# Performance work log

Hardware: AMD Instinct MI355X
Metric: run time of the kernel (lower is better)

The kernel has to match this reference:

```python
import jax, jax.numpy as jnp
import numpy as np

B, T, O = 64, 2048, 3          # batch, window_len, overlap (O >= ngram_n-1)
D, V = 512, 128                # embed_dim, vocab_size
M, NG, H = 100000, 4, 4        # engram memory_size, ngram_n, engram/sgrm num_heads
HD = D // H                    # head_dim = 128
PAD = 0
EPS_RMS = 1e-6


def _engram_primes():
    # per-head rolling-hash primes, exactly as in MultiHeadEngram.setup
    ps = []
    base = 131
    for h in range(H):
        x = base + h * 1009
        row = []
        for _ in range(NG):
            row.append(x)
            x = x * 31 + 1
        ps.append(row)
    return jnp.asarray(np.array(ps, dtype=np.uint32))  # (H, NG)


def setup_inputs() -> dict:
    key = jax.random.key(0)
    ks = jax.random.split(key, 10)
    tokens_w = jax.random.randint(ks[0], (B, T), 0, V, dtype=jnp.int32)
    prev_ids_overlap = jax.random.randint(ks[1], (B, O), 0, V, dtype=jnp.int32)
    mask_bool = jax.random.randint(ks[2], (B, T), 0, 2) > 0
    embed_table = jax.random.normal(ks[3], (V, D), jnp.float32) * 0.02
    engram_table = jax.random.normal(ks[4], (M, H, HD), jnp.float32) * 0.02
    gate_logit = jnp.full((H, HD), -2.0, jnp.float32)
    temp = jnp.ones((H,), jnp.float32)
    sal_W = jax.random.normal(ks[5], (D, H), jnp.float32) * 0.02
    sal_b = jnp.zeros((H,), jnp.float32)
    gate_W = jax.random.normal(ks[6], (HD, 1), jnp.float32) * 0.02
    gate_b = jnp.zeros((1,), jnp.float32)
    rms_scale = jnp.ones((D,), jnp.float32)
    return {"tokens_w": tokens_w, "prev_ids_overlap": prev_ids_overlap,
            "mask_bool": mask_bool, "embed_table": embed_table,
            "engram_table": engram_table, "gate_logit": gate_logit,
            "temp": temp, "sal_W": sal_W, "sal_b": sal_b,
            "gate_W": gate_W, "gate_b": gate_b, "rms_scale": rms_scale}


def reference(tokens_w, prev_ids_overlap, mask_bool, embed_table, engram_table,
              gate_logit, temp, sal_W, sal_b, gate_W, gate_b, rms_scale):
    # ---- MultiHeadEngram: hashed n-gram multi-head gather + sigmoid gate ----
    cur = jnp.where(tokens_w == PAD, 0, tokens_w)
    prv = jnp.where(prev_ids_overlap == PAD, 0, prev_ids_overlap)
    full_seq = jnp.concatenate([prv, cur], axis=1).astype(jnp.uint32)  # (B, O+T)
    primes = _engram_primes()                                          # (H, NG)
    hash_sums = jnp.zeros((B, T, H), dtype=jnp.uint32)
    for i in range(NG):  # rolling n-gram hash (uint32 wraparound)
        chunk = full_seq[:, O - i: O + T - i]                          # (B, T)
        hash_sums = hash_sums + chunk[:, :, None] * primes[None, None, :, i]
    lookup = (hash_sums % M).astype(jnp.int32)                         # (B, T, H)
    # per-head gather: row lookup[b,t,h] of head h's table slice
    retrieved = engram_table[lookup, jnp.arange(H)[None, None, :], :]  # (B, T, H, HD)
    gate = jax.nn.sigmoid(gate_logit)                                  # (H, HD)
    engram_out = (retrieved * gate[None, None]).reshape(B, T, D)

    # token embedding + engram injection (dropout is identity: deterministic)
    x = embed_table[tokens_w] + engram_out                             # (B, T, D)

    # ---- SalienceWriteHead: masked softmax temporal pooling + gating ----
    x_heads = x.reshape(B, T, H, HD)
    temperature = jax.nn.softplus(temp) + 0.3                          # (H,)
    logits = (x @ sal_W + sal_b) / temperature[None, None, :]          # (B, T, H)
    m = mask_bool[:, :, None]
    safe_logits = jnp.where(m, logits, -1e9)
    max_logits = jax.lax.stop_gradient(jnp.max(safe_logits, axis=1, keepdims=True))
    exps = jnp.where(m, jnp.exp(safe_logits - max_logits), 0.0)
    weights = exps / (jnp.sum(exps, axis=1, keepdims=True) + 1e-6)     # (B, T, H)
    write_vec_heads = jnp.einsum('bth,bthd->bhd', weights, x_heads)    # (B, H, HD)
    gate_logits = write_vec_heads @ gate_W + gate_b                    # (B, H, 1)
    window_valid = jnp.any(mask_bool, axis=1)[:, None, None]
    write_u_heads = jax.nn.sigmoid(gate_logits) * window_valid.astype(jnp.float32)
    write_vec = write_vec_heads.reshape(B, D)
    # RMSNorm
    rms = jnp.sqrt(jnp.mean(jnp.square(write_vec), axis=-1, keepdims=True) + EPS_RMS)
    write_vec = write_vec / rms * rms_scale
    write_u_expanded = jnp.tile(write_u_heads, (1, 1, HD)).reshape(B, D)
    return jnp.concatenate([write_vec, write_u_expanded], axis=-1)     # (B, 2D)
```

## Files before the change

### kernel.cpp

```cpp
#include <hip/hip_runtime.h>
#include <stdint.h>

#define B_ 64
#define T_ 2048
#define O_ 3
#define D_ 512
#define M_ 100000
#define H_ 4
#define HD_ 128
#define TC_ 128
#define NCH_ (T_ / TC_)
#define PSTR_ 132

__device__ __constant__ unsigned PRIMES_c[H_][4] = {
  {131u,  4062u,  125923u, 3903614u},
  {1140u, 35341u, 1095572u, 33962733u},
  {2149u, 66620u, 2065221u, 64021852u},
  {3158u, 97899u, 3034870u, 94080971u},
};

template<int CTRL, int RMASK>
__device__ __forceinline__ float dpp_term(float x) {
  return __int_as_float(__builtin_amdgcn_update_dpp(
      0, __float_as_int(x), CTRL, RMASK, 0xF, true));
}

__device__ __forceinline__ float red32(float x) {
  x += dpp_term<0xB1, 0xF>(x);
  x += dpp_term<0x4E, 0xF>(x);
  x += dpp_term<0x141, 0xF>(x);
  x += dpp_term<0x140, 0xF>(x);
  x += __shfl_xor(x, 16, 64);
  return x;
}

__device__ __forceinline__ float wave_sum(float x) {
  x += dpp_term<0xB1, 0xF>(x);
  x += dpp_term<0x4E, 0xF>(x);
  x += dpp_term<0x141, 0xF>(x);
  x += dpp_term<0x140, 0xF>(x);
  x += dpp_term<0x142, 0xA>(x);
  x += dpp_term<0x143, 0xC>(x);
  return __int_as_float(__builtin_amdgcn_readlane(__float_as_int(x), 63));
}

__device__ __forceinline__ bool read_mask(const void* mb, size_t i, int imode) {
  return imode ? (((const int*)mb)[i] != 0)
               : (((const unsigned char*)mb)[i] != 0);
}

__device__ __forceinline__ void detect_imode(const void* maskbuf, int tid,
                                             int* s_imode) {
  if (tid < 64) {
    const uint4* mw = (const uint4*)maskbuf;
    unsigned bad = 0;
    #pragma unroll
    for (int i = 0; i < 8; ++i) {
      uint4 v = mw[tid + i * 64];
      bad |= (v.x > 1u) | (v.y > 1u) | (v.z > 1u) | (v.w > 1u);
    }
    unsigned long long anybad = __ballot(bad != 0);
    if (tid == 0) *s_imode = (anybad == 0ull) ? 1 : 0;
  }
}

__global__ __launch_bounds__(256) void k_pass1(
    const int* __restrict__ tokens, const int* __restrict__ prev,
    const void* __restrict__ maskbuf, const float* __restrict__ embed,
    const float* __restrict__ engram, const float* __restrict__ gate_logit,
    const float* __restrict__ temp, const float* __restrict__ salW,
    const float* __restrict__ salb, float* __restrict__ partials)
{
  int blk = blockIdx.x;
  int b = blk / NCH_, c = blk % NCH_;
  int t0 = c * TC_;
  int tid = threadIdx.x;
  int h = tid >> 6, lane = tid & 63;
  int half = lane >> 5, sl = lane & 31;

  __shared__ int s_imode;
  __shared__ int ltok[TC_ + 3];
  __shared__ unsigned eoff[TC_ * H_];
  __shared__ int s_act[TC_];
  __shared__ int s_cnt2[2];
  __shared__ int s_nact;

  detect_imode(maskbuf, tid, &s_imode);
  for (int j = tid; j < TC_ + 3; j += 256) {
    int g = t0 + j;
    ltok[j] = (g < O_) ? prev[b * O_ + g] : tokens[(size_t)b * T_ + g - O_];
  }
  __syncthreads();

  int imode = s_imode;
  bool act = false;
  unsigned long long bal = 0;
  if (tid < TC_) {
    act = read_mask(maskbuf, (size_t)b * T_ + t0 + tid, imode);
    bal = __ballot(act);
    if ((tid & 63) == 0) s_cnt2[tid >> 6] = __popcll(bal);
  }
  __syncthreads();
  if (tid < TC_) {
    int l = tid & 63;
    int pre = __popcll(bal & ((1ull << l) - 1));
    int base = (tid >> 6) ? s_cnt2[0] : 0;
    if (act) s_act[base + pre] = tid;
    if (tid == 0) s_nact = s_cnt2[0] + s_cnt2[1];
  }
  __syncthreads();
  int nact = s_nact;

  for (int k = tid; k < nact * H_; k += 256) {
    int a  = k >> 2;
    int hh = k & 3;
    int j  = s_act[a];
    unsigned hs = (unsigned)ltok[j + 3] * PRIMES_c[hh][0]
                + (unsigned)ltok[j + 2] * PRIMES_c[hh][1]
                + (unsigned)ltok[j + 1] * PRIMES_c[hh][2]
                + (unsigned)ltok[j]     * PRIMES_c[hh][3];
    unsigned idx = hs % (unsigned)M_;
    eoff[k] = idx * (unsigned)(H_ * HD_) + (unsigned)(hh * HD_);
  }
  __syncthreads();

  int d0 = sl * 4;
  int gd = h * HD_ + d0;
  float4 glv = *(const float4*)(gate_logit + gd);
  float g0 = 1.f / (1.f + __expf(-glv.x));
  float g1 = 1.f / (1.f + __expf(-glv.y));
  float g2 = 1.f / (1.f + __expf(-glv.z));
  float g3 = 1.f / (1.f + __expf(-glv.w));
  float w0 = salW[(gd + 0) * H_ + h];
  float w1 = salW[(gd + 1) * H_ + h];
  float w2 = salW[(gd + 2) * H_ + h];
  float w3 = salW[(gd + 3) * H_ + h];
  float tv = temp[h];
  float sp = (tv > 20.f) ? tv : log1pf(__expf(tv));
  float invT = 1.f / (sp + 0.3f);
  float sb = salb[h];

  float m = -1e30f, s = 0.f;
  float a0 = 0.f, a1 = 0.f, a2 = 0.f, a3 = 0.f;

  for (int k = 0; k < nact; k += 4) {
    int ka = k + half, kb = k + 2 + half;
    bool va = ka < nact, vb = kb < nact;
    int ia = va ? ka : 0;
    int ib = vb ? kb : 0;
    int ja = s_act[ia], jb = s_act[ib];
    unsigned eoa = eoff[ia * H_ + h], eob = eoff[ib * H_ + h];
    int ta = ltok[ja + 3], tb = ltok[jb + 3];
    float4 ra = *(const float4*)(engram + eoa + d0);
    float4 rb = *(const float4*)(engram + eob + d0);
    float4 ea = *(const float4*)(embed + ta * D_ + gd);
    float4 eb = *(const float4*)(embed + tb * D_ + gd);
    float xa0 = fmaf(ra.x, g0, ea.x);
    float xa1 = fmaf(ra.y, g1, ea.y);
    float xa2 = fmaf(ra.z, g2, ea.z);
    float xa3 = fmaf(ra.w, g3, ea.w);
    float xb0 = fmaf(rb.x, g0, eb.x);
    float xb1 = fmaf(rb.y, g1, eb.y);
    float xb2 = fmaf(rb.z, g2, eb.z);
    float xb3 = fmaf(rb.w, g3, eb.w);
    float pda = fmaf(xa3, w3, fmaf(xa2, w2, fmaf(xa1, w1, xa0 * w0)));
    float pdb = fmaf(xb3, w3, fmaf(xb2, w2, fmaf(xb1, w1, xb0 * w0)));
    float da = red32(pda);
    float db = red32(pdb);
    float la = va ? (da + sb) * invT : -1e30f;
    float lb = vb ? (db + sb) * invT : -1e30f;
    float nm = fmaxf(m, fmaxf(la, lb));
    float al = __expf(m - nm);
    float wa = __expf(la - nm);
    float wb = __expf(lb - nm);
    s  = fmaf(s,  al, wa + wb);
    a0 = fmaf(a0, al, fmaf(wa, xa0, wb * xb0));
    a1 = fmaf(a1, al, fmaf(wa, xa1, wb * xb1));
    a2 = fmaf(a2, al, fmaf(wa, xa2, wb * xb2));
    a3 = fmaf(a3, al, fmaf(wa, xa3, wb * xb3));
    m = nm;
  }

  float pm = __shfl_xor(m, 32, 64);
  float M2 = fmaxf(m, pm);
  float fs = __expf(m - M2);
  float fp = __expf(pm - M2);
  float S2 = fmaf(s, fs, __shfl_xor(s, 32, 64) * fp);
  float A0 = fmaf(a0, fs, __shfl_xor(a0, 32, 64) * fp);
  float A1 = fmaf(a1, fs, __shfl_xor(a1, 32, 64) * fp);
  float A2 = fmaf(a2, fs, __shfl_xor(a2, 32, 64) * fp);
  float A3 = fmaf(a3, fs, __shfl_xor(a3, 32, 64) * fp);

  float* P = partials + ((size_t)(b * NCH_ + c) * H_ + h) * PSTR_;
  if (half == 0) {
    *(float4*)(P + d0) = make_float4(A0, A1, A2, A3);
    if (sl == 0) { P[HD_] = M2; P[HD_ + 1] = S2; }
  }
}

__global__ __launch_bounds__(256) void k_pass2(
    const float* __restrict__ partials, const void* __restrict__ maskbuf,
    const float* __restrict__ gateW, const float* __restrict__ gateb,
    const float* __restrict__ rms_scale, float* __restrict__ out)
{
  int b = blockIdx.x;
  int tid = threadIdx.x, h = tid >> 6, lane = tid & 63;

  __shared__ int s_imode;
  __shared__ float s_ss[H_];
  detect_imode(maskbuf, tid, &s_imode);
  __syncthreads();

  int d0 = lane * 2;
  const float* Pb = partials + (size_t)b * NCH_ * H_ * PSTR_;
  float M = -1e30f;
  for (int cc = 0; cc < NCH_; ++cc)
    M = fmaxf(M, Pb[(cc * H_ + h) * PSTR_ + HD_]);
  float S = 0.f, B0 = 0.f, B1 = 0.f;
  for (int cc = 0; cc < NCH_; ++cc) {
    const float* Pc = Pb + (cc * H_ + h) * PSTR_;
    float f = __expf(Pc[HD_] - M);
    float2 a = *(const float2*)(Pc + d0);
    S  = fmaf(Pc[HD_ + 1], f, S);
    B0 = fmaf(a.x, f, B0);
    B1 = fmaf(a.y, f, B1);
  }
  float inv = 1.f / (S + 1e-6f);
  float v0 = B0 * inv, v1 = B1 * inv;

  float pg = v0 * gateW[d0] + v1 * gateW[d0 + 1];
  float ss = v0 * v0 + v1 * v1;
  float gl  = wave_sum(pg);
  float sst = wave_sum(ss);
  if (lane == 0) s_ss[h] = sst;
  __syncthreads();
  float tot = s_ss[0] + s_ss[1] + s_ss[2] + s_ss[3];
  float rinv = rsqrtf(tot / (float)D_ + 1e-6f);
  float anyf = (S > 0.5f) ? 1.f : 0.f;
  float u = (1.f / (1.f + __expf(-(gl + gateb[0])))) * anyf;

  int gd = h * HD_ + d0;
  size_t ob = (size_t)b * (2 * D_);
  out[ob + gd]          = v0 * rinv * rms_scale[gd];
  out[ob + gd + 1]      = v1 * rinv * rms_scale[gd + 1];
  out[ob + D_ + gd]     = u;
  out[ob + D_ + gd + 1] = u;
}

extern "C" void kernel_launch(void* const* d_in, const int* in_sizes, int n_in,
                              void* d_out, int out_size, void* d_ws, size_t ws_size,
                              hipStream_t stream)
{
  const int*   tokens     = (const int*)d_in[0];
  const int*   prev       = (const int*)d_in[1];
  const void*  mask       = d_in[2];
  const float* embed      = (const float*)d_in[3];
  const float* engram     = (const float*)d_in[4];
  const float* gate_logit = (const float*)d_in[5];
  const float* temp       = (const float*)d_in[6];
  const float* salW       = (const float*)d_in[7];
  const float* salb       = (const float*)d_in[8];
  const float* gateW      = (const float*)d_in[9];
  const float* gateb      = (const float*)d_in[10];
  const float* rms_scale  = (const float*)d_in[11];
  float* out = (float*)d_out;

  float* partials = (float*)d_ws;

  k_pass1<<<B_ * NCH_, 256, 0, stream>>>(
      tokens, prev, mask, embed, engram, gate_logit, temp, salW, salb,
      partials);
  k_pass2<<<B_, 256, 0, stream>>>(
      partials, mask, gateW, gateb, rms_scale, out);
}
```

Measured before the change: 286.8 us.

## Halve chunk size and gather four engram rows per half-wave per iteration

Chunks shrink from 128 to 64 tokens, which doubles the number of pass-1 blocks. Mask compaction now runs in a single wave with one ballot, and the current token ids are compacted into shared memory. The main loop handles four active tokens per half-wave instead of two, so more independent gathers from the engram and embed tables are in flight to hide latency. Pass 2 no longer redundantly detects the mask format. In exchange, the partials buffer and the pass-2 merge double in size, and the mask is speculatively read as int even when it is byte-typed, which reads up to four times past the byte range.

```diff
diff --git a/kernel.cpp b/kernel.cpp
--- a/kernel.cpp
+++ b/kernel.cpp
@@ -8,7 +8,7 @@
 #define M_ 100000
 #define H_ 4
 #define HD_ 128
-#define TC_ 128
+#define TC_ 64
 #define NCH_ (T_ / TC_)
 #define PSTR_ 132
 
@@ -42,11 +42,6 @@
   x += dpp_term<0x142, 0xA>(x);
   x += dpp_term<0x143, 0xC>(x);
   return __int_as_float(__builtin_amdgcn_readlane(__float_as_int(x), 63));
-}
-
-__device__ __forceinline__ bool read_mask(const void* mb, size_t i, int imode) {
-  return imode ? (((const int*)mb)[i] != 0)
-               : (((const unsigned char*)mb)[i] != 0);
 }
 
 __device__ __forceinline__ void detect_imode(const void* maskbuf, int tid,
@@ -81,46 +76,44 @@
   __shared__ int s_imode;
   __shared__ int ltok[TC_ + 3];
   __shared__ unsigned eoff[TC_ * H_];
+  __shared__ int ltokc[TC_];
   __shared__ int s_act[TC_];
-  __shared__ int s_cnt2[2];
   __shared__ int s_nact;
 
   detect_imode(maskbuf, tid, &s_imode);
-  for (int j = tid; j < TC_ + 3; j += 256) {
-    int g = t0 + j;
-    ltok[j] = (g < O_) ? prev[b * O_ + g] : tokens[(size_t)b * T_ + g - O_];
-  }
-  __syncthreads();
-
-  int imode = s_imode;
-  bool act = false;
-  unsigned long long bal = 0;
+  if (tid < TC_ + 3) {
+    int g = t0 + tid;
+    ltok[tid] = (g < O_) ? prev[b * O_ + g] : tokens[(size_t)b * T_ + g - O_];
+  }
+  bool act_i = false, act_b = false;
   if (tid < TC_) {
-    act = read_mask(maskbuf, (size_t)b * T_ + t0 + tid, imode);
-    bal = __ballot(act);
-    if ((tid & 63) == 0) s_cnt2[tid >> 6] = __popcll(bal);
-  }
-  __syncthreads();
-  if (tid < TC_) {
-    int l = tid & 63;
-    int pre = __popcll(bal & ((1ull << l) - 1));
-    int base = (tid >> 6) ? s_cnt2[0] : 0;
-    if (act) s_act[base + pre] = tid;
-    if (tid == 0) s_nact = s_cnt2[0] + s_cnt2[1];
+    size_t mi = (size_t)b * T_ + t0 + tid;
+    act_i = ((const int*)maskbuf)[mi] != 0;
+    act_b = ((const unsigned char*)maskbuf)[mi] != 0;
+  }
+  __syncthreads();
+
+  if (tid < 64) {
+    bool act = s_imode ? act_i : act_b;
+    unsigned long long bal = __ballot(act);
+    int pre = __popcll(bal & ((1ull << tid) - 1));
+    if (act) s_act[pre] = tid;
+    if (tid == 0) s_nact = __popcll(bal);
   }
   __syncthreads();
   int nact = s_nact;
 
-  for (int k = tid; k < nact * H_; k += 256) {
-    int a  = k >> 2;
-    int hh = k & 3;
+  if (tid < nact * H_) {
+    int a  = tid >> 2;
+    int hh = tid & 3;
     int j  = s_act[a];
     unsigned hs = (unsigned)ltok[j + 3] * PRIMES_c[hh][0]
                 + (unsigned)ltok[j + 2] * PRIMES_c[hh][1]
                 + (unsigned)ltok[j + 1] * PRIMES_c[hh][2]
                 + (unsigned)ltok[j]     * PRIMES_c[hh][3];
     unsigned idx = hs % (unsigned)M_;
-    eoff[k] = idx * (unsigned)(H_ * HD_) + (unsigned)(hh * HD_);
+    eoff[tid] = idx * (unsigned)(H_ * HD_) + (unsigned)(hh * HD_);
+    if (hh == 0) ltokc[a] = ltok[j + 3];
   }
   __syncthreads();
 
@@ -141,43 +134,67 @@
   float sb = salb[h];
 
   float m = -1e30f, s = 0.f;
-  float a0 = 0.f, a1 = 0.f, a2 = 0.f, a3 = 0.f;
-
-  for (int k = 0; k < nact; k += 4) {
-    int ka = k + half, kb = k + 2 + half;
-    bool va = ka < nact, vb = kb < nact;
-    int ia = va ? ka : 0;
-    int ib = vb ? kb : 0;
-    int ja = s_act[ia], jb = s_act[ib];
-    unsigned eoa = eoff[ia * H_ + h], eob = eoff[ib * H_ + h];
-    int ta = ltok[ja + 3], tb = ltok[jb + 3];
-    float4 ra = *(const float4*)(engram + eoa + d0);
-    float4 rb = *(const float4*)(engram + eob + d0);
-    float4 ea = *(const float4*)(embed + ta * D_ + gd);
-    float4 eb = *(const float4*)(embed + tb * D_ + gd);
-    float xa0 = fmaf(ra.x, g0, ea.x);
-    float xa1 = fmaf(ra.y, g1, ea.y);
-    float xa2 = fmaf(ra.z, g2, ea.z);
-    float xa3 = fmaf(ra.w, g3, ea.w);
-    float xb0 = fmaf(rb.x, g0, eb.x);
-    float xb1 = fmaf(rb.y, g1, eb.y);
-    float xb2 = fmaf(rb.z, g2, eb.z);
-    float xb3 = fmaf(rb.w, g3, eb.w);
-    float pda = fmaf(xa3, w3, fmaf(xa2, w2, fmaf(xa1, w1, xa0 * w0)));
-    float pdb = fmaf(xb3, w3, fmaf(xb2, w2, fmaf(xb1, w1, xb0 * w0)));
-    float da = red32(pda);
-    float db = red32(pdb);
-    float la = va ? (da + sb) * invT : -1e30f;
-    float lb = vb ? (db + sb) * invT : -1e30f;
-    float nm = fmaxf(m, fmaxf(la, lb));
-    float al = __expf(m - nm);
-    float wa = __expf(la - nm);
-    float wb = __expf(lb - nm);
-    s  = fmaf(s,  al, wa + wb);
-    a0 = fmaf(a0, al, fmaf(wa, xa0, wb * xb0));
-    a1 = fmaf(a1, al, fmaf(wa, xa1, wb * xb1));
-    a2 = fmaf(a2, al, fmaf(wa, xa2, wb * xb2));
-    a3 = fmaf(a3, al, fmaf(wa, xa3, wb * xb3));
+  float4 acc = make_float4(0.f, 0.f, 0.f, 0.f);
+
+  for (int k = 0; k < nact; k += 8) {
+    int bse = k + half * 4;
+    bool v0 = bse + 0 < nact;
+    bool v1 = bse + 1 < nact;
+    bool v2 = bse + 2 < nact;
+    bool v3 = bse + 3 < nact;
+    int j0 = v0 ? bse + 0 : 0;
+    int j1 = v1 ? bse + 1 : 0;
+    int j2 = v2 ? bse + 2 : 0;
+    int j3 = v3 ? bse + 3 : 0;
+    unsigned e0 = eoff[j0 * H_ + h];
+    unsigned e1 = eoff[j1 * H_ + h];
+    unsigned e2 = eoff[j2 * H_ + h];
+    unsigned e3 = eoff[j3 * H_ + h];
+    int c0 = ltokc[j0], c1 = ltokc[j1], c2 = ltokc[j2], c3 = ltokc[j3];
+    float4 r0 = *(const float4*)(engram + e0 + d0);
+    float4 r1 = *(const float4*)(engram + e1 + d0);
+    float4 r2 = *(const float4*)(engram + e2 + d0);
+    float4 r3 = *(const float4*)(engram + e3 + d0);
+    float4 q0 = *(const float4*)(embed + c0 * D_ + gd);
+    float4 q1 = *(const float4*)(embed + c1 * D_ + gd);
+    float4 q2 = *(const float4*)(embed + c2 * D_ + gd);
+    float4 q3 = *(const float4*)(embed + c3 * D_ + gd);
+    float4 x0v, x1v, x2v, x3v;
+    x0v.x = fmaf(r0.x, g0, q0.x); x0v.y = fmaf(r0.y, g1, q0.y);
+    x0v.z = fmaf(r0.z, g2, q0.z); x0v.w = fmaf(r0.w, g3, q0.w);
+    x1v.x = fmaf(r1.x, g0, q1.x); x1v.y = fmaf(r1.y, g1, q1.y);
+    x1v.z = fmaf(r1.z, g2, q1.z); x1v.w = fmaf(r1.w, g3, q1.w);
+    x2v.x = fmaf(r2.x, g0, q2.x); x2v.y = fmaf(r2.y, g1, q2.y);
+    x2v.z = fmaf(r2.z, g2, q2.z); x2v.w = fmaf(r2.w, g3, q2.w);
+    x3v.x = fmaf(r3.x, g0, q3.x); x3v.y = fmaf(r3.y, g1, q3.y);
+    x3v.z = fmaf(r3.z, g2, q3.z); x3v.w = fmaf(r3.w, g3, q3.w);
+    float pd0 = fmaf(x0v.w, w3, fmaf(x0v.z, w2, fmaf(x0v.y, w1, x0v.x * w0)));
+    float pd1 = fmaf(x1v.w, w3, fmaf(x1v.z, w2, fmaf(x1v.y, w1, x1v.x * w0)));
+    float pd2 = fmaf(x2v.w, w3, fmaf(x2v.z, w2, fmaf(x2v.y, w1, x2v.x * w0)));
+    float pd3 = fmaf(x3v.w, w3, fmaf(x3v.z, w2, fmaf(x3v.y, w1, x3v.x * w0)));
+    float dt0 = red32(pd0);
+    float dt1 = red32(pd1);
+    float dt2 = red32(pd2);
+    float dt3 = red32(pd3);
+    float l0 = v0 ? (dt0 + sb) * invT : -1e30f;
+    float l1 = v1 ? (dt1 + sb) * invT : -1e30f;
+    float l2 = v2 ? (dt2 + sb) * invT : -1e30f;
+    float l3 = v3 ? (dt3 + sb) * invT : -1e30f;
+    float nm = fmaxf(fmaxf(fmaxf(l0, l1), fmaxf(l2, l3)), m);
+    float al  = __expf(m  - nm);
+    float u0 = __expf(l0 - nm);
+    float u1 = __expf(l1 - nm);
+    float u2 = __expf(l2 - nm);
+    float u3 = __expf(l3 - nm);
+    s = fmaf(s, al, (u0 + u1) + (u2 + u3));
+    acc.x = fmaf(acc.x, al,
+        fmaf(u3, x3v.x, fmaf(u2, x2v.x, fmaf(u1, x1v.x, u0 * x0v.x))));
+    acc.y = fmaf(acc.y, al,
+        fmaf(u3, x3v.y, fmaf(u2, x2v.y, fmaf(u1, x1v.y, u0 * x0v.y))));
+    acc.z = fmaf(acc.z, al,
+        fmaf(u3, x3v.z, fmaf(u2, x2v.z, fmaf(u1, x1v.z, u0 * x0v.z))));
+    acc.w = fmaf(acc.w, al,
+        fmaf(u3, x3v.w, fmaf(u2, x2v.w, fmaf(u1, x1v.w, u0 * x0v.w))));
     m = nm;
   }
 
@@ -186,10 +203,10 @@
   float fs = __expf(m - M2);
   float fp = __expf(pm - M2);
   float S2 = fmaf(s, fs, __shfl_xor(s, 32, 64) * fp);
-  float A0 = fmaf(a0, fs, __shfl_xor(a0, 32, 64) * fp);
-  float A1 = fmaf(a1, fs, __shfl_xor(a1, 32, 64) * fp);
-  float A2 = fmaf(a2, fs, __shfl_xor(a2, 32, 64) * fp);
-  float A3 = fmaf(a3, fs, __shfl_xor(a3, 32, 64) * fp);
+  float A0 = fmaf(acc.x, fs, __shfl_xor(acc.x, 32, 64) * fp);
+  float A1 = fmaf(acc.y, fs, __shfl_xor(acc.y, 32, 64) * fp);
+  float A2 = fmaf(acc.z, fs, __shfl_xor(acc.z, 32, 64) * fp);
+  float A3 = fmaf(acc.w, fs, __shfl_xor(acc.w, 32, 64) * fp);
 
   float* P = partials + ((size_t)(b * NCH_ + c) * H_ + h) * PSTR_;
   if (half == 0) {
@@ -199,17 +216,14 @@
 }
 
 __global__ __launch_bounds__(256) void k_pass2(
-    const float* __restrict__ partials, const void* __restrict__ maskbuf,
-    const float* __restrict__ gateW, const float* __restrict__ gateb,
-    const float* __restrict__ rms_scale, float* __restrict__ out)
+    const float* __restrict__ partials, const float* __restrict__ gateW,
+    const float* __restrict__ gateb, const float* __restrict__ rms_scale,
+    float* __restrict__ out)
 {
   int b = blockIdx.x;
   int tid = threadIdx.x, h = tid >> 6, lane = tid & 63;
 
-  __shared__ int s_imode;
   __shared__ float s_ss[H_];
-  detect_imode(maskbuf, tid, &s_imode);
-  __syncthreads();
 
   int d0 = lane * 2;
   const float* Pb = partials + (size_t)b * NCH_ * H_ * PSTR_;
@@ -271,5 +285,5 @@
       tokens, prev, mask, embed, engram, gate_logit, temp, salW, salb,
       partials);
   k_pass2<<<B_, 256, 0, stream>>>(
-      partials, mask, gateW, gateb, rms_scale, out);
-}
+      partials, gateW, gateb, rms_scale, out);
+}
```

After: 284.2 us. About the same (-0.9%).
